# Kernel optimization log

Measured on AMD Instinct MI355X. Metric: run time of the kernel, lower is better.

The kernel has to match this reference:

```python
import jax, jax.numpy as jnp
from jax import lax
import numpy as np

B, T, I, H, L = 64, 512, 256, 768, 2


def setup_inputs() -> dict:
    key = jax.random.key(0)
    ks = jax.random.split(key, 1 + 4 * L)
    s = 1.0 / np.sqrt(H)
    inp = {"x": jax.random.normal(ks[0], (B, T, I), dtype=jnp.float32)}
    for l in range(L):
        in_dim = I if l == 0 else H
        k0, k1, k2, k3 = ks[1 + 4 * l: 5 + 4 * l]
        inp[f"w_ih{l}"] = jax.random.uniform(k0, (4 * H, in_dim), jnp.float32, -s, s)
        inp[f"w_hh{l}"] = jax.random.uniform(k1, (4 * H, H), jnp.float32, -s, s)
        inp[f"b_ih{l}"] = jax.random.uniform(k2, (4 * H,), jnp.float32, -s, s)
        inp[f"b_hh{l}"] = jax.random.uniform(k3, (4 * H,), jnp.float32, -s, s)
    return inp


def _lstm_layer(xs, w_ih, w_hh, b_ih, b_hh):
    # xs: [B,T,in]; precompute input projections for all timesteps at once
    gx = jnp.einsum('bti,gi->btg', xs, w_ih) + b_ih  # [B,T,4H]
    h0 = jnp.zeros((xs.shape[0], H), xs.dtype)
    c0 = jnp.zeros((xs.shape[0], H), xs.dtype)

    def step(carry, gx_t):
        h, c = carry
        g = gx_t + h @ w_hh.T + b_hh  # [B,4H]
        i_g, f_g, g_g, o_g = jnp.split(g, 4, axis=-1)  # PyTorch gate order i,f,g,o
        i_g = jax.nn.sigmoid(i_g)
        f_g = jax.nn.sigmoid(f_g)
        g_g = jnp.tanh(g_g)
        o_g = jax.nn.sigmoid(o_g)
        c = f_g * c + i_g * g_g
        h = o_g * jnp.tanh(c)
        return (h, c), h

    (h, c), ys = lax.scan(step, (h0, c0), jnp.swapaxes(gx, 0, 1))  # scan over T
    return jnp.swapaxes(ys, 0, 1), h, c  # [B,T,H], [B,H], [B,H]


def reference(x, w_ih0, w_hh0, b_ih0, b_hh0, w_ih1, w_hh1, b_ih1, b_hh1):
    params = [(w_ih0, w_hh0, b_ih0, b_hh0), (w_ih1, w_hh1, b_ih1, b_hh1)]
    hs, cs = [], []
    ys = x
    for (w_ih, w_hh, b_ih, b_hh) in params:
        ys, h, c = _lstm_layer(ys, w_ih, w_hh, b_ih, b_hh)
        hs.append(h)
        cs.append(c)
    return ys, (tuple(hs), tuple(cs))
```

## Files before the change

kernel.cpp:

```cpp
#include <hip/hip_runtime.h>
#include <math.h>


#define B_   64
#define T_   512
#define I_   256
#define H_   768
#define G4H  3072

constexpr size_t BTH = (size_t)B_ * T_ * H_;
constexpr size_t BH  = (size_t)B_ * H_;

using f16_t = _Float16;
using f16x8 = __attribute__((ext_vector_type(8))) _Float16;
using f32x4 = __attribute__((ext_vector_type(4))) float;
typedef unsigned long long u64;

#define MFMA(a, b, c) __builtin_amdgcn_mfma_f32_16x16x32_f16((a), (b), (c), 0, 0, 0)

#define SLOT_STRIDE 98304
#define RING_SLOTS  16
#define RING_BYTES  (RING_SLOTS * SLOT_STRIDE)

#define SMEM_BYTES 132224

__global__ void k_packW(const float* __restrict__ src, f16_t* __restrict__ dst,
                        int K, int KC, int total) {
  int i = blockIdx.x * blockDim.x + threadIdx.x;
  int stride = gridDim.x * blockDim.x;
  for (; i < total; i += stride) {
    int e = i & 7;
    int lane = (i >> 3) & 63;
    int rest = i >> 9;
    int kc = rest % KC;
    int ptile = rest / KC;
    int p = ptile * 16 + (lane & 15);
    int k = kc * 32 + (lane >> 4) * 8 + e;
    int r = (p & 3) * H_ + (p >> 2);
    dst[i] = (f16_t)src[(size_t)r * K + k];
  }
}

__global__ void k_packX(const float* __restrict__ x, f16_t* __restrict__ dst) {
  int i = blockIdx.x * blockDim.x + threadIdx.x;
  int stride = gridDim.x * blockDim.x;
  const int total = 4 * T_ * 8 * 64 * 8;
  for (; i < total; i += stride) {
    int e = i & 7;
    int lane = (i >> 3) & 63;
    int kc = (i >> 9) & 7;
    int t = (i >> 12) & 511;
    int mtile = i >> 21;
    int b = mtile * 16 + (lane & 15);
    int k = kc * 32 + (lane >> 4) * 8 + e;
    dst[i] = (f16_t)x[((size_t)b * T_ + t) * I_ + k];
  }
}

__global__ void k_bias(const float* __restrict__ bih, const float* __restrict__ bhh,
                       float* __restrict__ bsum) {
  int p = blockIdx.x * blockDim.x + threadIdx.x;
  if (p < G4H) {
    int r = (p & 3) * H_ + (p >> 2);
    bsum[p] = bih[r] + bhh[r];
  }
}

__global__ void k_zero(int4* __restrict__ d, int n) {
  int stride = gridDim.x * blockDim.x;
  for (int i = blockIdx.x * blockDim.x + threadIdx.x; i < n; i += stride)
    d[i] = make_int4(0, 0, 0, 0);
}

__device__ __forceinline__ float sigf(float v) {
  return __builtin_amdgcn_rcpf(1.0f + __builtin_amdgcn_exp2f(v * -1.44269504f));
}
__device__ __forceinline__ float tanhf_fast(float v) {
  return 2.0f * __builtin_amdgcn_rcpf(1.0f + __builtin_amdgcn_exp2f(v * -2.88539008f)) - 1.0f;
}

__device__ __forceinline__ u64 ld_q(const u64* p) {
  return __hip_atomic_load(p, __ATOMIC_RELAXED, __HIP_MEMORY_SCOPE_AGENT);
}
__device__ __forceinline__ unsigned ld_flag(const int* p) {
  return (unsigned)__hip_atomic_load(p, __ATOMIC_RELAXED, __HIP_MEMORY_SCOPE_AGENT);
}

__device__ __forceinline__ void wait_super(const int* p, unsigned tagv) {
  for (;;) {
    if (ld_flag(p) == tagv) return;
    __builtin_amdgcn_s_sleep(1);
  }
}

template <int KCW>
__device__ __forceinline__ void load_mfma(const char* sb, const int (&bA)[KCW],
                                          const f16_t* wl0, const f16_t* wl1,
                                          f32x4& a00, f32x4& a01, f32x4& a10,
                                          f32x4& a11) {
  u64 vA[KCW][2], vB[KCW][2];
#pragma unroll
  for (int i = 0; i < KCW; ++i) {
    const u64* p = (const u64*)(sb + bA[i]);
    vA[i][0] = ld_q(p);
    vA[i][1] = ld_q(p + 64);
    vB[i][0] = ld_q(p + 16);
    vB[i][1] = ld_q(p + 80);
  }
#pragma unroll
  for (int i = 0; i < KCW; ++i) {
    union { u64 q[2]; f16x8 f; } cA, cB;
    cA.q[0] = vA[i][0]; cA.q[1] = vA[i][1];
    cB.q[0] = vB[i][0]; cB.q[1] = vB[i][1];
    f16x8 w0 = *(const f16x8*)(wl0 + (size_t)i * 512);
    f16x8 w1 = *(const f16x8*)(wl1 + (size_t)i * 512);
    a00 = MFMA(cA.f, w0, a00);
    a01 = MFMA(cA.f, w1, a01);
    a10 = MFMA(cB.f, w0, a10);
    a11 = MFMA(cB.f, w1, a11);
  }
}

__device__ __forceinline__ void run_agg(const int* __restrict__ flags,
                                        int* __restrict__ sup) {
  if ((threadIdx.x >> 6) != 0) return;
  const int lane = threadIdx.x & 63;
  for (int t = 0; t < T_; ++t) {
    const int* f = flags + (size_t)t * 128 * 4;
    const unsigned want = (unsigned)(t + 1);
    for (;;) {
      unsigned v0 = ld_flag(f + lane * 4);
      unsigned v1 = (lane < 32) ? ld_flag(f + (64 + lane) * 4) : want;
      if (__all((v0 == want) & (v1 == want))) break;
    }
    asm volatile("s_waitcnt vmcnt(0)" ::: "memory");
    if (lane == 0)
      __hip_atomic_store(sup + (size_t)t * 4, (int)want, __ATOMIC_RELAXED,
                         __HIP_MEMORY_SCOPE_AGENT);
  }
}

template <int KCW, bool IS_L1>
__device__ __forceinline__ void run_layer(
    int ws, const f16_t* __restrict__ Xf, const f16_t* __restrict__ Wihf,
    const f16_t* __restrict__ Whhf, const float* __restrict__ bsum,
    char* __restrict__ ring0c, char* __restrict__ ring1c,
    int* __restrict__ flag0, int* __restrict__ flag1,
    int* __restrict__ sup0, int* __restrict__ sup1,
    float* __restrict__ out, char* smem) {
  f16_t* WL = (f16_t*)smem;
  float (*pre)[64][33] = (float (*)[64][33])(smem + 98304);
  float* bsL = (float*)(smem + 132096);

  const int tid = threadIdx.x;
  const int wave = tid >> 6, lane = tid & 63;
  const int kg = wave & 3, mg = wave >> 2;
  const int laneo = lane * 8;
  const int pt0 = ws * 2, m0 = mg * 2;
  const int l15 = lane & 15, l4 = lane >> 4;

  if (tid < 32) bsL[tid] = bsum[ws * 32 + tid];

  if (mg == 0) {
    const f16_t* src;
    int KC, kc0;
    if constexpr (!IS_L1) {
      if (kg == 0) { src = Wihf; KC = 8;  kc0 = 0; }
      else         { src = Whhf; KC = 24; kc0 = (kg - 1) * 8; }
    } else {
      if (kg < 2)  { src = Wihf; KC = 24; kc0 = kg * 12; }
      else         { src = Whhf; KC = 24; kc0 = (kg - 2) * 12; }
    }
#pragma unroll
    for (int p = 0; p < 2; ++p)
#pragma unroll
      for (int i = 0; i < KCW; ++i)
        *(uint4*)(WL + ((size_t)((kg * 2 + p) * KCW + i)) * 512 + laneo) =
            *(const uint4*)(src + ((size_t)(pt0 + p) * KC + kc0 + i) * 512 + laneo);
  }

  int kcs = 0;
  if constexpr (!IS_L1) kcs = (kg - 1) * 8;
  else                  kcs = (kg < 2) ? kg * 12 : (kg - 2) * 12;

  int bA[KCW];
#pragma unroll
  for (int i = 0; i < KCW; ++i)
    bA[i] = ((kcs + i) * 4 + l4) * 1024 + (m0 * 16 + l15) * 8;

  float c_reg = 0.f;
  const int u = tid & 7, b = tid >> 3;
  const int j = ws * 8 + u;
  char* myringc = IS_L1 ? ring1c : ring0c;
  int* myflag = IS_L1 ? flag1 : flag0;
  const f16_t* wl0 = WL + (size_t)(kg * 2) * KCW * 512 + laneo;
  const f16_t* wl1 = wl0 + (size_t)KCW * 512;

  __syncthreads();

  for (int t = 0; t < T_; ++t) {
    f32x4 a00 = {0.f, 0.f, 0.f, 0.f};
    f32x4 a01 = {0.f, 0.f, 0.f, 0.f};
    f32x4 a10 = {0.f, 0.f, 0.f, 0.f};
    f32x4 a11 = {0.f, 0.f, 0.f, 0.f};

    if constexpr (!IS_L1) {
      if (kg == 0) {
        if (mg == 1 && t >= RING_SLOTS)
          wait_super(sup1 + (size_t)(t - RING_SLOTS) * 4,
                     (unsigned)(t - RING_SLOTS + 1));
        const f16_t* A0 = Xf + ((size_t)m0 * T_ + t) * 4096 + laneo;
        const f16_t* A1 = A0 + (size_t)T_ * 4096;
#pragma unroll
        for (int i = 0; i < KCW; ++i) {
          f16x8 x0 = *(const f16x8*)(A0 + (size_t)i * 512);
          f16x8 x1 = *(const f16x8*)(A1 + (size_t)i * 512);
          f16x8 w0 = *(const f16x8*)(wl0 + (size_t)i * 512);
          f16x8 w1 = *(const f16x8*)(wl1 + (size_t)i * 512);
          a00 = MFMA(x0, w0, a00);
          a01 = MFMA(x0, w1, a01);
          a10 = MFMA(x1, w0, a10);
          a11 = MFMA(x1, w1, a11);
        }
      } else if (t >= 1) {
        wait_super(sup0 + (size_t)(t - 1) * 4, (unsigned)t);
        const char* sb = ring0c + (size_t)((t - 1) & (RING_SLOTS - 1)) * SLOT_STRIDE;
        load_mfma<KCW>(sb, bA, wl0, wl1, a00, a01, a10, a11);
      }
    } else {
      const int srcstep = (kg < 2) ? t : t - 1;
      if (srcstep >= 0) {
        const unsigned tg = (unsigned)(srcstep + 1);
        wait_super(((kg < 2) ? sup0 : sup1) + (size_t)srcstep * 4, tg);
        const char* sb = ((kg < 2) ? ring0c : ring1c) +
                         (size_t)(srcstep & (RING_SLOTS - 1)) * SLOT_STRIDE;
        load_mfma<KCW>(sb, bA, wl0, wl1, a00, a01, a10, a11);
      }
    }

#pragma unroll
    for (int r = 0; r < 4; ++r) {
      pre[kg][m0 * 16 + l4 * 4 + r][l15]           = a00[r];
      pre[kg][m0 * 16 + l4 * 4 + r][16 + l15]      = a01[r];
      pre[kg][m0 * 16 + 16 + l4 * 4 + r][l15]      = a10[r];
      pre[kg][m0 * 16 + 16 + l4 * 4 + r][16 + l15] = a11[r];
    }
    __syncthreads();

    float h;
    {
      float g0 = pre[0][b][4 * u + 0] + pre[1][b][4 * u + 0] + pre[2][b][4 * u + 0] + pre[3][b][4 * u + 0] + bsL[4 * u + 0];
      float g1 = pre[0][b][4 * u + 1] + pre[1][b][4 * u + 1] + pre[2][b][4 * u + 1] + pre[3][b][4 * u + 1] + bsL[4 * u + 1];
      float g2 = pre[0][b][4 * u + 2] + pre[1][b][4 * u + 2] + pre[2][b][4 * u + 2] + pre[3][b][4 * u + 2] + bsL[4 * u + 2];
      float g3 = pre[0][b][4 * u + 3] + pre[1][b][4 * u + 3] + pre[2][b][4 * u + 3] + pre[3][b][4 * u + 3] + bsL[4 * u + 3];
      float ig = sigf(g0), fg = sigf(g1), gg = tanhf_fast(g2), og = sigf(g3);
      c_reg = fg * c_reg + ig * gg;
      h = og * tanhf_fast(c_reg);

      unsigned hb = (unsigned)__builtin_bit_cast(unsigned short, (f16_t)h);
      unsigned n1 = (unsigned)__shfl((int)hb, lane + 1);
      unsigned n2 = (unsigned)__shfl((int)hb, lane + 2);
      unsigned n3 = (unsigned)__shfl((int)hb, lane + 3);
      if ((u & 3) == 0) {
        u64 val = (u64)(hb | (n1 << 16)) | ((u64)(n2 | (n3 << 16)) << 32);
        u64* dst = (u64*)(myringc +
                          (size_t)(t & (RING_SLOTS - 1)) * SLOT_STRIDE +
                          (size_t)ws * 1024 + (u >> 2) * 512 + (size_t)b * 8);
        __hip_atomic_store(dst, val, __ATOMIC_RELAXED, __HIP_MEMORY_SCOPE_AGENT);
      }
    }
    asm volatile("s_waitcnt vmcnt(0)" ::: "memory");
    __syncthreads();
    if (tid == 0)
      __hip_atomic_store(myflag + ((size_t)t * 128 + ws) * 4, t + 1,
                         __ATOMIC_RELAXED, __HIP_MEMORY_SCOPE_AGENT);

    if constexpr (IS_L1) {
      out[((size_t)b * T_ + t) * H_ + j] = h;
      if (t == T_ - 1) {
        out[BTH + BH + (size_t)b * H_ + j] = h;
        out[BTH + 3 * BH + (size_t)b * H_ + j] = c_reg;
      }
    } else {
      if (t == T_ - 1) {
        out[BTH + (size_t)b * H_ + j] = h;
        out[BTH + 2 * BH + (size_t)b * H_ + j] = c_reg;
      }
    }
  }
}

__launch_bounds__(512, 1)
__global__ void k_lstm(const f16_t* __restrict__ Xf,
                       const f16_t* __restrict__ Wih0f, const f16_t* __restrict__ Whh0f,
                       const f16_t* __restrict__ Wih1f, const f16_t* __restrict__ Whh1f,
                       const float* __restrict__ bsum0, const float* __restrict__ bsum1,
                       char* __restrict__ ring0c, char* __restrict__ ring1c,
                       int* __restrict__ flag0, int* __restrict__ flag1,
                       int* __restrict__ sup0, int* __restrict__ sup1,
                       float* __restrict__ out) {
  extern __shared__ char smem[];
  const int wg = blockIdx.x;
  if (wg < 96)
    run_layer<8, false>(wg, Xf, Wih0f, Whh0f, bsum0, ring0c, ring1c,
                        flag0, flag1, sup0, sup1, out, smem);
  else if (wg < 192)
    run_layer<12, true>(wg - 96, Xf, Wih1f, Whh1f, bsum1, ring0c, ring1c,
                        flag0, flag1, sup0, sup1, out, smem);
  else if (wg == 192)
    run_agg(flag0, sup0);
  else
    run_agg(flag1, sup1);
}

extern "C" void kernel_launch(void* const* d_in, const int* in_sizes, int n_in,
                              void* d_out, int out_size, void* d_ws, size_t ws_size,
                              hipStream_t stream) {
  const float* x    = (const float*)d_in[0];
  const float* wih0 = (const float*)d_in[1];
  const float* whh0 = (const float*)d_in[2];
  const float* bih0 = (const float*)d_in[3];
  const float* bhh0 = (const float*)d_in[4];
  const float* wih1 = (const float*)d_in[5];
  const float* whh1 = (const float*)d_in[6];
  const float* bih1 = (const float*)d_in[7];
  const float* bhh1 = (const float*)d_in[8];
  float* out = (float*)d_out;

  char* base = (char*)d_ws;
  size_t off = 0;
  auto take = [&](size_t bytes) -> char* {
    char* r = base + off;
    off = (off + bytes + 255) & ~(size_t)255;
    return r;
  };
  f16_t* Wih0f = (f16_t*)take((size_t)G4H * I_ * 2);
  f16_t* Whh0f = (f16_t*)take((size_t)G4H * H_ * 2);
  f16_t* Wih1f = (f16_t*)take((size_t)G4H * H_ * 2);
  f16_t* Whh1f = (f16_t*)take((size_t)G4H * H_ * 2);
  f16_t* Xf    = (f16_t*)take((size_t)4 * T_ * 8 * 64 * 8 * 2);
  float* bsum0 = (float*)take((size_t)G4H * 4);
  float* bsum1 = (float*)take((size_t)G4H * 4);
  char* ring0c = take(RING_BYTES);
  char* ring1c = take(RING_BYTES);
  const size_t flagBytes = (size_t)T_ * 128 * 16;
  const size_t supBytes  = (size_t)T_ * 16;
  char* fl = take(2 * flagBytes + 2 * supBytes);
  int* flag0 = (int*)fl;
  int* flag1 = flag0 + (size_t)T_ * 128 * 4;
  int* sup0  = flag1 + (size_t)T_ * 128 * 4;
  int* sup1  = sup0 + (size_t)T_ * 4;
  const size_t zeroBytes = 2 * flagBytes + 2 * supBytes;

  hipFuncSetAttribute(reinterpret_cast<const void*>(k_lstm),
                      hipFuncAttributeMaxDynamicSharedMemorySize, SMEM_BYTES);

  k_packW<<<768, 256, 0, stream>>>(wih0, Wih0f, I_, 8, G4H * I_);
  k_packW<<<2048, 256, 0, stream>>>(whh0, Whh0f, H_, 24, G4H * H_);
  k_packW<<<2048, 256, 0, stream>>>(wih1, Wih1f, H_, 24, G4H * H_);
  k_packW<<<2048, 256, 0, stream>>>(whh1, Whh1f, H_, 24, G4H * H_);
  k_packX<<<4096, 256, 0, stream>>>(x, Xf);
  k_bias<<<12, 256, 0, stream>>>(bih0, bhh0, bsum0);
  k_bias<<<12, 256, 0, stream>>>(bih1, bhh1, bsum1);
  k_zero<<<520, 256, 0, stream>>>((int4*)fl, (int)(zeroBytes / 16));

  k_lstm<<<194, 512, SMEM_BYTES, stream>>>(Xf, Wih0f, Whh0f, Wih1f, Whh1f,
                                           bsum0, bsum1, ring0c, ring1c,
                                           flag0, flag1, sup0, sup1, out);
}
```

Baseline: 2.208 ms.

## Use per-wave 16-bit completion flags and 16-byte packed hidden-state ring writes

Each wave now publishes its own 16-bit step flag right after its hidden-state stores drain, so the per-step workgroup barrier before flag publication is no longer on the critical path. The aggregator polls packed 64-bit words, each covering the eight waves of one workgroup, instead of one flag per workgroup. Hidden-state ring writes are repacked so one lane stores 8 halves (two 64-bit stores) per row, with the reader's load offsets changed to match. This aims to cut cross-workgroup signalling latency per timestep. The risk is that 16-bit flags wrap or race, and the barrier moved to the end of the step could still serialize the work.

New measurement: 2.773 ms. 1.26x slower.

```diff
diff --git a/kernel.cpp b/kernel.cpp
--- a/kernel.cpp
+++ b/kernel.cpp
@@ -21,6 +21,8 @@
 #define SLOT_STRIDE 98304
 #define RING_SLOTS  16
 #define RING_BYTES  (RING_SLOTS * SLOT_STRIDE)
+
+constexpr size_t WF_BYTES = (size_t)T_ * 96 * 16;
 
 #define SMEM_BYTES 132224
 
@@ -103,9 +105,9 @@
   for (int i = 0; i < KCW; ++i) {
     const u64* p = (const u64*)(sb + bA[i]);
     vA[i][0] = ld_q(p);
-    vA[i][1] = ld_q(p + 64);
-    vB[i][0] = ld_q(p + 16);
-    vB[i][1] = ld_q(p + 80);
+    vA[i][1] = ld_q(p + 1);
+    vB[i][0] = ld_q(p + 32);
+    vB[i][1] = ld_q(p + 33);
   }
 #pragma unroll
   for (int i = 0; i < KCW; ++i) {
@@ -121,21 +123,21 @@
   }
 }
 
-__device__ __forceinline__ void run_agg(const int* __restrict__ flags,
+__device__ __forceinline__ void run_agg(const u64* __restrict__ wf,
                                         int* __restrict__ sup) {
   if ((threadIdx.x >> 6) != 0) return;
   const int lane = threadIdx.x & 63;
   for (int t = 0; t < T_; ++t) {
-    const int* f = flags + (size_t)t * 128 * 4;
-    const unsigned want = (unsigned)(t + 1);
+    const u64* f = wf + (size_t)t * 192;
+    const u64 want = (u64)(unsigned)(t + 1) * 0x0001000100010001ULL;
     for (;;) {
-      unsigned v0 = ld_flag(f + lane * 4);
-      unsigned v1 = (lane < 32) ? ld_flag(f + (64 + lane) * 4) : want;
-      if (__all((v0 == want) & (v1 == want))) break;
-    }
-    asm volatile("s_waitcnt vmcnt(0)" ::: "memory");
+      u64 a = ld_q(f + lane);
+      u64 b = ld_q(f + 64 + lane);
+      u64 c = ld_q(f + 128 + lane);
+      if (__all((int)((a == want) & (b == want) & (c == want)))) break;
+    }
     if (lane == 0)
-      __hip_atomic_store(sup + (size_t)t * 4, (int)want, __ATOMIC_RELAXED,
+      __hip_atomic_store(sup + (size_t)t * 4, t + 1, __ATOMIC_RELAXED,
                          __HIP_MEMORY_SCOPE_AGENT);
   }
 }
@@ -145,7 +147,7 @@
     int ws, const f16_t* __restrict__ Xf, const f16_t* __restrict__ Wihf,
     const f16_t* __restrict__ Whhf, const float* __restrict__ bsum,
     char* __restrict__ ring0c, char* __restrict__ ring1c,
-    int* __restrict__ flag0, int* __restrict__ flag1,
+    u64* __restrict__ wf0, u64* __restrict__ wf1,
     int* __restrict__ sup0, int* __restrict__ sup1,
     float* __restrict__ out, char* smem) {
   f16_t* WL = (f16_t*)smem;
@@ -186,13 +188,13 @@
   int bA[KCW];
 #pragma unroll
   for (int i = 0; i < KCW; ++i)
-    bA[i] = ((kcs + i) * 4 + l4) * 1024 + (m0 * 16 + l15) * 8;
+    bA[i] = ((kcs + i) * 4 + l4) * 1024 + (m0 * 16 + l15) * 16;
 
   float c_reg = 0.f;
   const int u = tid & 7, b = tid >> 3;
   const int j = ws * 8 + u;
   char* myringc = IS_L1 ? ring1c : ring0c;
-  int* myflag = IS_L1 ? flag1 : flag0;
+  u64* mywf = IS_L1 ? wf1 : wf0;
   const f16_t* wl0 = WL + (size_t)(kg * 2) * KCW * 512 + laneo;
   const f16_t* wl1 = wl0 + (size_t)KCW * 512;
 
@@ -258,22 +260,32 @@
       h = og * tanhf_fast(c_reg);
 
       unsigned hb = (unsigned)__builtin_bit_cast(unsigned short, (f16_t)h);
-      unsigned n1 = (unsigned)__shfl((int)hb, lane + 1);
-      unsigned n2 = (unsigned)__shfl((int)hb, lane + 2);
-      unsigned n3 = (unsigned)__shfl((int)hb, lane + 3);
-      if ((u & 3) == 0) {
-        u64 val = (u64)(hb | (n1 << 16)) | ((u64)(n2 | (n3 << 16)) << 32);
+      const int gbase = lane & ~7;
+      unsigned s0 = (unsigned)__shfl((int)hb, gbase + 0);
+      unsigned s1 = (unsigned)__shfl((int)hb, gbase + 1);
+      unsigned s2 = (unsigned)__shfl((int)hb, gbase + 2);
+      unsigned s3 = (unsigned)__shfl((int)hb, gbase + 3);
+      unsigned s4 = (unsigned)__shfl((int)hb, gbase + 4);
+      unsigned s5 = (unsigned)__shfl((int)hb, gbase + 5);
+      unsigned s6 = (unsigned)__shfl((int)hb, gbase + 6);
+      unsigned s7 = (unsigned)__shfl((int)hb, gbase + 7);
+      if (u == 0) {
+        u64 lo = (u64)(s0 | (s1 << 16)) | ((u64)(s2 | (s3 << 16)) << 32);
+        u64 hi = (u64)(s4 | (s5 << 16)) | ((u64)(s6 | (s7 << 16)) << 32);
         u64* dst = (u64*)(myringc +
                           (size_t)(t & (RING_SLOTS - 1)) * SLOT_STRIDE +
-                          (size_t)ws * 1024 + (u >> 2) * 512 + (size_t)b * 8);
-        __hip_atomic_store(dst, val, __ATOMIC_RELAXED, __HIP_MEMORY_SCOPE_AGENT);
+                          (size_t)ws * 1024 + (size_t)b * 16);
+        __hip_atomic_store(dst,     lo, __ATOMIC_RELAXED, __HIP_MEMORY_SCOPE_AGENT);
+        __hip_atomic_store(dst + 1, hi, __ATOMIC_RELAXED, __HIP_MEMORY_SCOPE_AGENT);
       }
     }
     asm volatile("s_waitcnt vmcnt(0)" ::: "memory");
-    __syncthreads();
-    if (tid == 0)
-      __hip_atomic_store(myflag + ((size_t)t * 128 + ws) * 4, t + 1,
-                         __ATOMIC_RELAXED, __HIP_MEMORY_SCOPE_AGENT);
+    if (lane == 0) {
+      unsigned short* fp =
+          (unsigned short*)((char*)mywf + ((size_t)t * 96 + ws) * 16) + wave;
+      __hip_atomic_store(fp, (unsigned short)(t + 1), __ATOMIC_RELAXED,
+                         __HIP_MEMORY_SCOPE_AGENT);
+    }
 
     if constexpr (IS_L1) {
       out[((size_t)b * T_ + t) * H_ + j] = h;
@@ -287,6 +299,7 @@
         out[BTH + 2 * BH + (size_t)b * H_ + j] = c_reg;
       }
     }
+    __syncthreads();
   }
 }
 
@@ -296,21 +309,21 @@
                        const f16_t* __restrict__ Wih1f, const f16_t* __restrict__ Whh1f,
                        const float* __restrict__ bsum0, const float* __restrict__ bsum1,
                        char* __restrict__ ring0c, char* __restrict__ ring1c,
-                       int* __restrict__ flag0, int* __restrict__ flag1,
+                       u64* __restrict__ wf0, u64* __restrict__ wf1,
                        int* __restrict__ sup0, int* __restrict__ sup1,
                        float* __restrict__ out) {
   extern __shared__ char smem[];
   const int wg = blockIdx.x;
   if (wg < 96)
     run_layer<8, false>(wg, Xf, Wih0f, Whh0f, bsum0, ring0c, ring1c,
-                        flag0, flag1, sup0, sup1, out, smem);
+                        wf0, wf1, sup0, sup1, out, smem);
   else if (wg < 192)
     run_layer<12, true>(wg - 96, Xf, Wih1f, Whh1f, bsum1, ring0c, ring1c,
-                        flag0, flag1, sup0, sup1, out, smem);
+                        wf0, wf1, sup0, sup1, out, smem);
   else if (wg == 192)
-    run_agg(flag0, sup0);
+    run_agg(wf0, sup0);
   else
-    run_agg(flag1, sup1);
+    run_agg(wf1, sup1);
 }
 
 extern "C" void kernel_launch(void* const* d_in, const int* in_sizes, int n_in,
@@ -343,14 +356,13 @@
   float* bsum1 = (float*)take((size_t)G4H * 4);
   char* ring0c = take(RING_BYTES);
   char* ring1c = take(RING_BYTES);
-  const size_t flagBytes = (size_t)T_ * 128 * 16;
-  const size_t supBytes  = (size_t)T_ * 16;
-  char* fl = take(2 * flagBytes + 2 * supBytes);
-  int* flag0 = (int*)fl;
-  int* flag1 = flag0 + (size_t)T_ * 128 * 4;
-  int* sup0  = flag1 + (size_t)T_ * 128 * 4;
-  int* sup1  = sup0 + (size_t)T_ * 4;
-  const size_t zeroBytes = 2 * flagBytes + 2 * supBytes;
+  const size_t supBytes = (size_t)T_ * 16;
+  char* fl = take(2 * WF_BYTES + 2 * supBytes);
+  u64* wf0 = (u64*)fl;
+  u64* wf1 = (u64*)(fl + WF_BYTES);
+  int* sup0 = (int*)(fl + 2 * WF_BYTES);
+  int* sup1 = sup0 + (size_t)T_ * 4;
+  const size_t zeroBytes = 2 * WF_BYTES + 2 * supBytes;
 
   hipFuncSetAttribute(reinterpret_cast<const void*>(k_lstm),
                       hipFuncAttributeMaxDynamicSharedMemorySize, SMEM_BYTES);
@@ -366,5 +378,5 @@
 
   k_lstm<<<194, 512, SMEM_BYTES, stream>>>(Xf, Wih0f, Whh0f, Wih1f, Whh1f,
                                            bsum0, bsum1, ring0c, ring1c,
-                                           flag0, flag1, sup0, sup1, out);
-}
+                                           wf0, wf1, sup0, sup1, out);
+}
```
